# Performance work log

Hardware: AMD Instinct MI355X
Metric: run time of the kernel (lower is better)

Reference implementation:

```python
import jax, jax.numpy as jnp
import numpy as np
import math

HID = 512
HEADS = 8
DK = HID // HEADS
B, S, T = 8, 4096, 512


def setup_inputs() -> dict:
    key = jax.random.key(0)
    ks = jax.random.split(key, 12)
    scale = 0.02
    inp = {
        "inputs": jax.random.normal(ks[0], (B, S, HID), dtype=jnp.float32),
        "targets": jax.random.normal(ks[1], (B, T, HID), dtype=jnp.float32),
        "mask": jnp.ones((B, S), dtype=bool),
        "Wq": jax.random.normal(ks[2], (HID, HID), dtype=jnp.float32) * scale,
        "bq": jnp.zeros((HID,), dtype=jnp.float32),
        "Wk": jax.random.normal(ks[3], (HID, HID), dtype=jnp.float32) * scale,
        "bk": jnp.zeros((HID,), dtype=jnp.float32),
        "Wv": jax.random.normal(ks[4], (HID, HID), dtype=jnp.float32) * scale,
        "bv": jnp.zeros((HID,), dtype=jnp.float32),
        "Wo": jax.random.normal(ks[5], (HID, HID), dtype=jnp.float32) * scale,
        "bo": jnp.zeros((HID,), dtype=jnp.float32),
    }
    return inp


def reference(inputs, targets, mask, Wq, bq, Wk, bk, Wv, bv, Wo, bo):
    # PoolingFunction(method='multihead-attention'), dropout=0 (identity),
    # hidden_size == output_size so mapping_function is identity.
    b, t, h = targets.shape
    s = inputs.shape[1]
    Q = (targets @ Wq.T + bq).reshape(b, t, HEADS, DK)
    K = (inputs @ Wk.T + bk).reshape(b, s, HEADS, DK)
    V = (inputs @ Wv.T + bv).reshape(b, s, HEADS, DK)
    # scores: b x heads x tgt x seq (same math as (Q*K).sum(-1)/sqrt(d_k))
    e = jnp.einsum('bthd,bshd->bhts', Q, K) / math.sqrt(DK)
    neg = (1.0 - mask.astype(jnp.float32)) * -1e20  # b x s
    e = e + neg[:, None, None, :]
    a = jax.nn.softmax(e, axis=-1)  # softmax over seq dim
    ctx = jnp.einsum('bhts,bshd->bthd', a, V).reshape(b, t, h)
    return ctx @ Wo.T + bo
```

## Files before the change

### kernel.cpp

```cpp
#include <hip/hip_runtime.h>
#include <hip/hip_bf16.h>
#include <cstdint>
#include <cstddef>

#define HIDN   512
#define NHEADS 8
#define BATCH  8
#define SLEN   4096
#define TLEN   512
#define SSPLIT 4
#define SCHUNK (SLEN / SSPLIT)
#define SCL2   0.18033688f

typedef __attribute__((ext_vector_type(8))) short   bf16x8;
typedef __attribute__((ext_vector_type(4))) float   f32x4;
typedef unsigned short u16;
typedef unsigned int   u32;

__device__ __forceinline__ u32 pkbf(float a, float b) {
    __hip_bfloat162 h = __float22bfloat162_rn(float2{a, b});
    union { __hip_bfloat162 h; u32 u; } un; un.h = h; return un.u;
}
__device__ __forceinline__ u32 pk2(float a, float b) {
    union { float f; u32 u; } ua, ub; ua.f = a; ub.f = b;
    return __builtin_amdgcn_perm(ub.u + 0x8000u, ua.u + 0x8000u, 0x07060302u);
}
__device__ __forceinline__ void gload_lds16(const u16* g, u16* l) {
    __builtin_amdgcn_global_load_lds(
        (const __attribute__((address_space(1))) u32*)g,
        (__attribute__((address_space(3))) u32*)l, 16, 0, 0);
}

__global__ __launch_bounds__(256) void cvt_all(
    const float* __restrict__ X, const float* __restrict__ Tg,
    const float* __restrict__ Wq, const float* __restrict__ Wk,
    const float* __restrict__ Wv, const float* __restrict__ Wo,
    const int* __restrict__ mask,
    u16* __restrict__ Xc, u16* __restrict__ Tc, u16* __restrict__ Wc,
    float* __restrict__ negf)
{
    int i4 = blockIdx.x * 256 + threadIdx.x;
    if (i4 >= 4980736) {
        int off = i4 - 4980736;
        int4 mv = ((const int4*)mask)[off];
        float4 nv;
        nv.x = mv.x ? 0.f : -1e30f; nv.y = mv.y ? 0.f : -1e30f;
        nv.z = mv.z ? 0.f : -1e30f; nv.w = mv.w ? 0.f : -1e30f;
        ((float4*)negf)[off] = nv;
        return;
    }
    const float* s; u16* d; long off;
    if (i4 < 4194304)      { s = X;  d = Xc; off = i4; }
    else if (i4 < 4718592) { s = Tg; d = Tc; off = i4 - 4194304; }
    else {
        int wi = i4 - 4718592; int widx = wi >> 16;
        s = (widx == 0) ? Wq : (widx == 1) ? Wk : (widx == 2) ? Wv : Wo;
        d = Wc + widx * 262144; off = wi & 65535;
    }
    float4 v = *(const float4*)(s + off * 4);
    uint2 o; o.x = pkbf(v.x, v.y); o.y = pkbf(v.z, v.w);
    *(uint2*)(d + off * 4) = o;
}

template<int MODE, int SEQ>
__global__ __launch_bounds__(256)
void gemm_bf16(const u16* __restrict__ A, const u16* __restrict__ Bw,
               const float* __restrict__ bias, void* __restrict__ Yv)
{
    __shared__ u16 As[128 * 32];
    __shared__ u16 Bs[128 * 32];
    const int tid = threadIdx.x;
    const int lane = tid & 63, w = tid >> 6;
    const int m = lane & 15, qd = lane >> 4;
    const int wm = w >> 1, wn = w & 1;
    const int m0 = blockIdx.y * 128, n0 = blockIdx.x * 128;

    f32x4 acc[4][4];
#pragma unroll
    for (int i = 0; i < 4; ++i)
#pragma unroll
        for (int j = 0; j < 4; ++j) acc[i][j] = (f32x4){0.f, 0.f, 0.f, 0.f};

    for (int k0 = 0; k0 < HIDN; k0 += 32) {
#pragma unroll
        for (int r = 0; r < 2; ++r) {
            const int f = tid + r * 256;
            const int row = f >> 2, c8 = (f & 3) * 8;
            const int fb = f & ~63;
            gload_lds16(A  + (size_t)(m0 + row) * HIDN + k0 + c8, As + fb * 8);
            gload_lds16(Bw + (size_t)(n0 + row) * HIDN + k0 + c8, Bs + fb * 8);
        }
        __syncthreads();
        bf16x8 af[4], bf[4];
#pragma unroll
        for (int t = 0; t < 4; ++t) {
            af[t] = *(bf16x8*)&As[(64 * wm + 16 * t + m) * 32 + 8 * qd];
            bf[t] = *(bf16x8*)&Bs[(64 * wn + 16 * t + m) * 32 + 8 * qd];
        }
#pragma unroll
        for (int ti = 0; ti < 4; ++ti)
#pragma unroll
            for (int tj = 0; tj < 4; ++tj)
                acc[ti][tj] = __builtin_amdgcn_mfma_f32_16x16x32_bf16(
                    af[ti], bf[tj], acc[ti][tj], 0, 0, 0);
        __syncthreads();
    }

#pragma unroll
    for (int ti = 0; ti < 4; ++ti) {
        const int gr0 = m0 + 64 * wm + 16 * ti + 4 * qd;
#pragma unroll
        for (int tj = 0; tj < 4; ++tj) {
            const int gcol = n0 + 64 * wn + 16 * tj + m;
            const float bv = bias[gcol];
            if (MODE == 0) {
                float* Y = (float*)Yv;
#pragma unroll
                for (int i = 0; i < 4; ++i)
                    Y[(size_t)(gr0 + i) * HIDN + gcol] = acc[ti][tj][i] + bv;
            } else {
                u16* Y = (u16*)Yv;
                const int b = gr0 / SEQ, h = gcol >> 6, d = gcol & 63;
                const int r = gr0 & (SEQ - 1);
                uint2 o;
                o.x = pkbf(acc[ti][tj][0] + bv, acc[ti][tj][1] + bv);
                o.y = pkbf(acc[ti][tj][2] + bv, acc[ti][tj][3] + bv);
                *(uint2*)&Y[(((size_t)(b * 8 + h)) * 64 + d) * SEQ + r] = o;
            }
        }
    }
}

template<int SEQ>
__global__ __launch_bounds__(256)
void gemm_wxT(const u16* __restrict__ Wm, const u16* __restrict__ X,
              const float* __restrict__ bias, u16* __restrict__ Y)
{
    __shared__ u16 As[128 * 32];
    __shared__ u16 Bs[128 * 32];
    const int tid = threadIdx.x;
    const int lane = tid & 63, w = tid >> 6;
    const int m = lane & 15, qd = lane >> 4;
    const int wm = w >> 1, wn = w & 1;
    const int m0 = blockIdx.y * 128, n0 = blockIdx.x * 128;

    f32x4 acc[4][4];
#pragma unroll
    for (int i = 0; i < 4; ++i)
#pragma unroll
        for (int j = 0; j < 4; ++j) acc[i][j] = (f32x4){0.f, 0.f, 0.f, 0.f};

    for (int k0 = 0; k0 < HIDN; k0 += 32) {
#pragma unroll
        for (int r = 0; r < 2; ++r) {
            const int f = tid + r * 256;
            const int row = f >> 2, c8 = (f & 3) * 8;
            const int fb = f & ~63;
            gload_lds16(Wm + (size_t)(m0 + row) * HIDN + k0 + c8, As + fb * 8);
            gload_lds16(X  + (size_t)(n0 + row) * HIDN + k0 + c8, Bs + fb * 8);
        }
        __syncthreads();
        bf16x8 af[4], bf[4];
#pragma unroll
        for (int t = 0; t < 4; ++t) {
            af[t] = *(bf16x8*)&As[(64 * wm + 16 * t + m) * 32 + 8 * qd];
            bf[t] = *(bf16x8*)&Bs[(64 * wn + 16 * t + m) * 32 + 8 * qd];
        }
#pragma unroll
        for (int ti = 0; ti < 4; ++ti)
#pragma unroll
            for (int tj = 0; tj < 4; ++tj)
                acc[ti][tj] = __builtin_amdgcn_mfma_f32_16x16x32_bf16(
                    af[ti], bf[tj], acc[ti][tj], 0, 0, 0);
        __syncthreads();
    }

#pragma unroll
    for (int ti = 0; ti < 4; ++ti) {
        const int o = m0 + 64 * wm + 16 * ti + 4 * qd;
        const float4 bv = *(const float4*)&bias[o];
        const int h = o >> 6, d0 = o & 63;
#pragma unroll
        for (int tj = 0; tj < 4; ++tj) {
            const int n = n0 + 64 * wn + 16 * tj + m;
            const int b = n / SEQ, r = n & (SEQ - 1);
            uint2 pk;
            pk.x = pkbf(acc[ti][tj][0] + bv.x, acc[ti][tj][1] + bv.y);
            pk.y = pkbf(acc[ti][tj][2] + bv.z, acc[ti][tj][3] + bv.w);
            *(uint2*)&Y[(((size_t)(b * 8 + h)) * SEQ + r) * 64 + d0] = pk;
        }
    }
}

__global__ __launch_bounds__(256, 2)
void attn_part(const u16* __restrict__ Q, const u16* __restrict__ K,
               const u16* __restrict__ Vt, const float* __restrict__ negf,
               float* __restrict__ Opart, float* __restrict__ lpart)
{
    __shared__ char Psh[32768];
    const int tid = threadIdx.x;
    const int lane = tid & 63, w = tid >> 6;
    const int m = lane & 15, qd = lane >> 4;
    const int ti = blockIdx.x, si = blockIdx.y, bh = blockIdx.z;
    const int b = bh >> 3;

    const u16* Qp = Q + ((size_t)bh * TLEN + ti * 256) * 64;
    const u16* Kp = K + (size_t)bh * SLEN * 64;
    const u16* Vp = Vt + (size_t)bh * 64 * SLEN;
    const float* np = negf + (size_t)b * SLEN;

    const int wb = w * 8192 + m * 128;
    int waddr[4], ra0[2], ra1[2];
#pragma unroll
    for (int st = 0; st < 4; ++st) waddr[st] = wb + (((4 * st + qd) ^ m) << 3);
#pragma unroll
    for (int ks = 0; ks < 2; ++ks) {
        const int u0 = 8 * ks + 2 * qd;
        ra0[ks] = wb + (((u0) ^ m) << 3);
        ra1[ks] = wb + (((u0 + 1) ^ m) << 3);
    }

    bf16x8 qf[4][2];
#pragma unroll
    for (int ts = 0; ts < 4; ++ts)
#pragma unroll
        for (int kh = 0; kh < 2; ++kh)
            qf[ts][kh] = *(const bf16x8*)(Qp + (64 * w + 16 * ts + m) * 64 +
                                          32 * kh + 8 * qd);

    f32x4 O[4][4];
#pragma unroll
    for (int ts = 0; ts < 4; ++ts)
#pragma unroll
        for (int dt = 0; dt < 4; ++dt) O[ts][dt] = (f32x4){0.f, 0.f, 0.f, 0.f};
    float lr[4] = {0.f, 0.f, 0.f, 0.f};

    const int s_beg = si * SCHUNK;
    const u16* kp = Kp + (size_t)(s_beg + m) * 64 + 8 * qd;
    const u16* vp0 = Vp + (size_t)m * SLEN + s_beg + 8 * qd;
    const u16* vp1 = vp0 + (size_t)16 * SLEN;
    const u16* vp2 = vp0 + (size_t)32 * SLEN;
    const u16* vp3 = vp0 + (size_t)48 * SLEN;
    const float* npp = np + s_beg + 4 * qd;

#pragma unroll 1
    for (int c = 0; c < SCHUNK; c += 64) {
        bf16x8 kf[4][2];
        kf[0][0] = *(const bf16x8*)(kp + 0);
        kf[0][1] = *(const bf16x8*)(kp + 32);
        kf[1][0] = *(const bf16x8*)(kp + 1024);
        kf[1][1] = *(const bf16x8*)(kp + 1056);
        kf[2][0] = *(const bf16x8*)(kp + 2048);
        kf[2][1] = *(const bf16x8*)(kp + 2080);
        kf[3][0] = *(const bf16x8*)(kp + 3072);
        kf[3][1] = *(const bf16x8*)(kp + 3104);
        float4 ng[4];
        ng[0] = *(const float4*)(npp + 0);
        ng[1] = *(const float4*)(npp + 16);
        ng[2] = *(const float4*)(npp + 32);
        ng[3] = *(const float4*)(npp + 48);
        bf16x8 vf[4][2];
        vf[0][0] = *(const bf16x8*)(vp0 + 0);
        vf[0][1] = *(const bf16x8*)(vp0 + 32);
        vf[1][0] = *(const bf16x8*)(vp1 + 0);
        vf[1][1] = *(const bf16x8*)(vp1 + 32);
        vf[2][0] = *(const bf16x8*)(vp2 + 0);
        vf[2][1] = *(const bf16x8*)(vp2 + 32);
        vf[3][0] = *(const bf16x8*)(vp3 + 0);
        vf[3][1] = *(const bf16x8*)(vp3 + 32);

#pragma unroll
        for (int ts = 0; ts < 4; ++ts) {
            f32x4 S[4];
#pragma unroll
            for (int st = 0; st < 4; ++st) {
                f32x4 cc = (f32x4){0.f, 0.f, 0.f, 0.f};
                cc = __builtin_amdgcn_mfma_f32_16x16x32_bf16(kf[st][0], qf[ts][0], cc, 0, 0, 0);
                cc = __builtin_amdgcn_mfma_f32_16x16x32_bf16(kf[st][1], qf[ts][1], cc, 0, 0, 0);
                S[st] = cc;
            }
            float ls = 0.f;
#pragma unroll
            for (int st = 0; st < 4; ++st) {
                const float p0 = exp2f(fmaf(S[st][0], SCL2, ng[st].x));
                const float p1 = exp2f(fmaf(S[st][1], SCL2, ng[st].y));
                const float p2 = exp2f(fmaf(S[st][2], SCL2, ng[st].z));
                const float p3 = exp2f(fmaf(S[st][3], SCL2, ng[st].w));
                ls += (p0 + p1) + (p2 + p3);
                *(uint2*)&Psh[waddr[st] + ts * 2048] =
                    make_uint2(pk2(p0, p1), pk2(p2, p3));
            }
            lr[ts] += ls;
#pragma unroll
            for (int ks = 0; ks < 2; ++ks) {
                const uint2 r0 = *(uint2*)&Psh[ra0[ks] + ts * 2048];
                const uint2 r1 = *(uint2*)&Psh[ra1[ks] + ts * 2048];
                union { uint4 u; bf16x8 v; } bu;
                bu.u = make_uint4(r0.x, r0.y, r1.x, r1.y);
                O[ts][0] = __builtin_amdgcn_mfma_f32_16x16x32_bf16(vf[0][ks], bu.v, O[ts][0], 0, 0, 0);
                O[ts][1] = __builtin_amdgcn_mfma_f32_16x16x32_bf16(vf[1][ks], bu.v, O[ts][1], 0, 0, 0);
                O[ts][2] = __builtin_amdgcn_mfma_f32_16x16x32_bf16(vf[2][ks], bu.v, O[ts][2], 0, 0, 0);
                O[ts][3] = __builtin_amdgcn_mfma_f32_16x16x32_bf16(vf[3][ks], bu.v, O[ts][3], 0, 0, 0);
            }
        }
        kp += 4096; vp0 += 64; vp1 += 64; vp2 += 64; vp3 += 64; npp += 64;
    }

#pragma unroll
    for (int ts = 0; ts < 4; ++ts) {
        float l = lr[ts];
        l += __shfl_xor(l, 16, 64);
        l += __shfl_xor(l, 32, 64);
        const int t = ti * 256 + 64 * w + 16 * ts + m;
        float* Ob = Opart + (((size_t)(si * 64 + bh)) * 512 + t) * 64;
#pragma unroll
        for (int dt = 0; dt < 4; ++dt)
            *(f32x4*)&Ob[16 * dt + 4 * qd] = O[ts][dt];
        if (qd == 0)
            lpart[((size_t)(si * 64 + bh)) * 512 + t] = l;
    }
}

__global__ __launch_bounds__(256)
void attn_combine(const float* __restrict__ Opart, const float* __restrict__ lpart,
                  u16* __restrict__ ctx)
{
    const int gid = blockIdx.x * 256 + threadIdx.x;
    const int d4 = gid & 15, t = (gid >> 4) & 511, bh = gid >> 13;
    const int b = bh >> 3, h = bh & 7;
    float4 o = {0.f, 0.f, 0.f, 0.f}; float l = 0.f;
#pragma unroll
    for (int si = 0; si < SSPLIT; ++si) {
        const size_t base = ((size_t)(si * 64 + bh)) * 512 + t;
        l += lpart[base];
        const float4 v = *(const float4*)(Opart + base * 64 + d4 * 4);
        o.x += v.x; o.y += v.y; o.z += v.z; o.w += v.w;
    }
    const float r = 1.f / l;
    uint2 pk; pk.x = pkbf(o.x * r, o.y * r); pk.y = pkbf(o.z * r, o.w * r);
    *(uint2*)&ctx[((size_t)(b * 512 + t)) * 512 + h * 64 + d4 * 4] = pk;
}

extern "C" void kernel_launch(void* const* d_in, const int* in_sizes, int n_in,
                              void* d_out, int out_size, void* d_ws, size_t ws_size,
                              hipStream_t stream)
{
    const float* inputs  = (const float*)d_in[0];
    const float* targets = (const float*)d_in[1];
    const int*   mask    = (const int*)d_in[2];
    const float* Wq = (const float*)d_in[3];
    const float* bq = (const float*)d_in[4];
    const float* Wk = (const float*)d_in[5];
    const float* bk = (const float*)d_in[6];
    const float* Wv = (const float*)d_in[7];
    const float* bv = (const float*)d_in[8];
    const float* Wo = (const float*)d_in[9];
    const float* bo = (const float*)d_in[10];

    char* ws = (char*)d_ws;
    u16*   Xc    = (u16*)(ws);
    u16*   Tc    = (u16*)(ws + 33554432);
    u16*   Wc    = (u16*)(ws + 37748736);
    float* negf  = (float*)(ws + 39845888);
    u16*   Qws   = (u16*)(ws + 39976960);
    u16*   Kws   = (u16*)(ws + 44171264);
    u16*   Vtws  = (u16*)(ws + 77725696);
    u16*   Cws   = (u16*)(ws + 111280128);
    float* Opart = (float*)(ws + 115474432);
    float* lpart = (float*)(ws + 149028864);

    cvt_all<<<19488, 256, 0, stream>>>(inputs, targets, Wq, Wk, Wv, Wo, mask,
                                       Xc, Tc, Wc, negf);

    gemm_wxT<TLEN><<<dim3(32, 4),  256, 0, stream>>>(Wc,          Tc, bq, Qws);
    gemm_wxT<SLEN><<<dim3(256, 4), 256, 0, stream>>>(Wc + 262144, Xc, bk, Kws);
    gemm_bf16<2, SLEN><<<dim3(4, 256), 256, 0, stream>>>(Xc, Wc + 524288, bv, Vtws);

    attn_part<<<dim3(2, SSPLIT, 64), 256, 0, stream>>>(Qws, Kws, Vtws, negf,
                                                       Opart, lpart);
    attn_combine<<<2048, 256, 0, stream>>>(Opart, lpart, Cws);

    gemm_bf16<0, TLEN><<<dim3(4, 32), 256, 0, stream>>>(Cws, Wc + 786432, bo,
                                                        (float*)d_out);
}
```

Baseline: 299.2 us.

## Fuse split-S attention and combine into one 1024-thread block with LDS reduction

New measurement: 351.2 us. 17.4% more time.

```diff
diff --git a/kernel.cpp b/kernel.cpp
--- a/kernel.cpp
+++ b/kernel.cpp
@@ -8,8 +8,6 @@
 #define BATCH  8
 #define SLEN   4096
 #define TLEN   512
-#define SSPLIT 4
-#define SCHUNK (SLEN / SSPLIT)
 #define SCL2   0.18033688f
 
 typedef __attribute__((ext_vector_type(8))) short   bf16x8;
@@ -192,50 +190,54 @@
     }
 }
 
-__global__ __launch_bounds__(256, 2)
-void attn_part(const u16* __restrict__ Q, const u16* __restrict__ K,
-               const u16* __restrict__ Vt, const float* __restrict__ negf,
-               float* __restrict__ Opart, float* __restrict__ lpart)
-{
-    __shared__ char Psh[32768];
+__global__ __launch_bounds__(1024, 4)
+void attn_fused(const u16* __restrict__ Q, const u16* __restrict__ K,
+                const u16* __restrict__ Vt, const float* __restrict__ negf,
+                u16* __restrict__ ctx)
+{
+    __shared__ char  Psh[16 * 4096];
+    __shared__ float comb[8][4][64][4];
+    __shared__ float lsh[4][32];
+
     const int tid = threadIdx.x;
     const int lane = tid & 63, w = tid >> 6;
+    const int sg = w >> 2, tw = w & 3;
     const int m = lane & 15, qd = lane >> 4;
-    const int ti = blockIdx.x, si = blockIdx.y, bh = blockIdx.z;
-    const int b = bh >> 3;
-
-    const u16* Qp = Q + ((size_t)bh * TLEN + ti * 256) * 64;
+    const int ti = blockIdx.x, bh = blockIdx.y;
+    const int b = bh >> 3, h = bh & 7;
+
+    const u16* Qp = Q + ((size_t)bh * TLEN + ti * 128) * 64;
     const u16* Kp = K + (size_t)bh * SLEN * 64;
     const u16* Vp = Vt + (size_t)bh * 64 * SLEN;
     const float* np = negf + (size_t)b * SLEN;
 
-    const int wb = w * 8192 + m * 128;
+    const int wb = w * 4096 + m * 128;
     int waddr[4], ra0[2], ra1[2];
 #pragma unroll
     for (int st = 0; st < 4; ++st) waddr[st] = wb + (((4 * st + qd) ^ m) << 3);
 #pragma unroll
     for (int ks = 0; ks < 2; ++ks) {
         const int u0 = 8 * ks + 2 * qd;
-        ra0[ks] = wb + (((u0) ^ m) << 3);
+        ra0[ks] = wb + ((u0 ^ m) << 3);
         ra1[ks] = wb + (((u0 + 1) ^ m) << 3);
     }
 
-    bf16x8 qf[4][2];
-#pragma unroll
-    for (int ts = 0; ts < 4; ++ts)
+    bf16x8 qf[2][2];
+#pragma unroll
+    for (int ts = 0; ts < 2; ++ts)
 #pragma unroll
         for (int kh = 0; kh < 2; ++kh)
-            qf[ts][kh] = *(const bf16x8*)(Qp + (64 * w + 16 * ts + m) * 64 +
+            qf[ts][kh] = *(const bf16x8*)(Qp + (tw * 32 + ts * 16 + m) * 64 +
                                           32 * kh + 8 * qd);
 
-    f32x4 O[4][4];
-#pragma unroll
-    for (int ts = 0; ts < 4; ++ts)
+    f32x4 O[2][4];
+#pragma unroll
+    for (int ts = 0; ts < 2; ++ts)
 #pragma unroll
         for (int dt = 0; dt < 4; ++dt) O[ts][dt] = (f32x4){0.f, 0.f, 0.f, 0.f};
-    float lr[4] = {0.f, 0.f, 0.f, 0.f};
-
-    const int s_beg = si * SCHUNK;
+    float lr[2] = {0.f, 0.f};
+
+    const int s_beg = sg * 1024;
     const u16* kp = Kp + (size_t)(s_beg + m) * 64 + 8 * qd;
     const u16* vp0 = Vp + (size_t)m * SLEN + s_beg + 8 * qd;
     const u16* vp1 = vp0 + (size_t)16 * SLEN;
@@ -244,7 +246,7 @@
     const float* npp = np + s_beg + 4 * qd;
 
 #pragma unroll 1
-    for (int c = 0; c < SCHUNK; c += 64) {
+    for (int c = 0; c < 1024; c += 64) {
         bf16x8 kf[4][2];
         kf[0][0] = *(const bf16x8*)(kp + 0);
         kf[0][1] = *(const bf16x8*)(kp + 32);
@@ -270,7 +272,7 @@
         vf[3][1] = *(const bf16x8*)(vp3 + 32);
 
 #pragma unroll
-        for (int ts = 0; ts < 4; ++ts) {
+        for (int ts = 0; ts < 2; ++ts) {
             f32x4 S[4];
 #pragma unroll
             for (int st = 0; st < 4; ++st) {
@@ -282,10 +284,10 @@
             float ls = 0.f;
 #pragma unroll
             for (int st = 0; st < 4; ++st) {
-                const float p0 = exp2f(fmaf(S[st][0], SCL2, ng[st].x));
-                const float p1 = exp2f(fmaf(S[st][1], SCL2, ng[st].y));
-                const float p2 = exp2f(fmaf(S[st][2], SCL2, ng[st].z));
-                const float p3 = exp2f(fmaf(S[st][3], SCL2, ng[st].w));
+                const float p0 = __builtin_amdgcn_exp2f(fmaf(S[st][0], SCL2, ng[st].x));
+                const float p1 = __builtin_amdgcn_exp2f(fmaf(S[st][1], SCL2, ng[st].y));
+                const float p2 = __builtin_amdgcn_exp2f(fmaf(S[st][2], SCL2, ng[st].z));
+                const float p3 = __builtin_amdgcn_exp2f(fmaf(S[st][3], SCL2, ng[st].w));
                 ls += (p0 + p1) + (p2 + p3);
                 *(uint2*)&Psh[waddr[st] + ts * 2048] =
                     make_uint2(pk2(p0, p1), pk2(p2, p3));
@@ -306,39 +308,53 @@
         kp += 4096; vp0 += 64; vp1 += 64; vp2 += 64; vp3 += 64; npp += 64;
     }
 
-#pragma unroll
-    for (int ts = 0; ts < 4; ++ts) {
+    float lt[2];
+#pragma unroll
+    for (int ts = 0; ts < 2; ++ts) {
         float l = lr[ts];
         l += __shfl_xor(l, 16, 64);
         l += __shfl_xor(l, 32, 64);
-        const int t = ti * 256 + 64 * w + 16 * ts + m;
-        float* Ob = Opart + (((size_t)(si * 64 + bh)) * 512 + t) * 64;
-#pragma unroll
-        for (int dt = 0; dt < 4; ++dt)
-            *(f32x4*)&Ob[16 * dt + 4 * qd] = O[ts][dt];
-        if (qd == 0)
-            lpart[((size_t)(si * 64 + bh)) * 512 + t] = l;
-    }
-}
-
-__global__ __launch_bounds__(256)
-void attn_combine(const float* __restrict__ Opart, const float* __restrict__ lpart,
-                  u16* __restrict__ ctx)
-{
-    const int gid = blockIdx.x * 256 + threadIdx.x;
-    const int d4 = gid & 15, t = (gid >> 4) & 511, bh = gid >> 13;
-    const int b = bh >> 3, h = bh & 7;
-    float4 o = {0.f, 0.f, 0.f, 0.f}; float l = 0.f;
-#pragma unroll
-    for (int si = 0; si < SSPLIT; ++si) {
-        const size_t base = ((size_t)(si * 64 + bh)) * 512 + t;
-        l += lpart[base];
-        const float4 v = *(const float4*)(Opart + base * 64 + d4 * 4);
-        o.x += v.x; o.y += v.y; o.z += v.z; o.w += v.w;
-    }
-    const float r = 1.f / l;
-    uint2 pk; pk.x = pkbf(o.x * r, o.y * r); pk.y = pkbf(o.z * r, o.w * r);
-    *(uint2*)&ctx[((size_t)(b * 512 + t)) * 512 + h * 64 + d4 * 4] = pk;
+        lt[ts] = l;
+    }
+#pragma unroll 1
+    for (int r = 1; r < 4; ++r) {
+        if (sg == r) {
+#pragma unroll
+            for (int ts = 0; ts < 2; ++ts)
+#pragma unroll
+                for (int dt = 0; dt < 4; ++dt)
+                    *(f32x4*)&comb[ts * 4 + dt][tw][lane][0] = O[ts][dt];
+            if (qd == 0) { lsh[tw][m] = lt[0]; lsh[tw][16 + m] = lt[1]; }
+        }
+        __syncthreads();
+        if (sg == 0) {
+#pragma unroll
+            for (int ts = 0; ts < 2; ++ts)
+#pragma unroll
+                for (int dt = 0; dt < 4; ++dt) {
+                    const f32x4 v = *(f32x4*)&comb[ts * 4 + dt][tw][lane][0];
+                    O[ts][dt] += v;
+                }
+            lt[0] += lsh[tw][m];
+            lt[1] += lsh[tw][16 + m];
+        }
+        __syncthreads();
+    }
+    if (sg == 0) {
+#pragma unroll
+        for (int ts = 0; ts < 2; ++ts) {
+            const float linv = 1.f / lt[ts];
+            const int t = ti * 128 + tw * 32 + ts * 16 + m;
+            u16* cp = ctx + ((size_t)(b * TLEN + t)) * HIDN + h * 64;
+#pragma unroll
+            for (int dt = 0; dt < 4; ++dt) {
+                uint2 o;
+                o.x = pkbf(O[ts][dt][0] * linv, O[ts][dt][1] * linv);
+                o.y = pkbf(O[ts][dt][2] * linv, O[ts][dt][3] * linv);
+                *(uint2*)&cp[16 * dt + 4 * qd] = o;
+            }
+        }
+    }
 }
 
 extern "C" void kernel_launch(void* const* d_in, const int* in_sizes, int n_in,
@@ -366,8 +382,6 @@
     u16*   Kws   = (u16*)(ws + 44171264);
     u16*   Vtws  = (u16*)(ws + 77725696);
     u16*   Cws   = (u16*)(ws + 111280128);
-    float* Opart = (float*)(ws + 115474432);
-    float* lpart = (float*)(ws + 149028864);
 
     cvt_all<<<19488, 256, 0, stream>>>(inputs, targets, Wq, Wk, Wv, Wo, mask,
                                        Xc, Tc, Wc, negf);
@@ -376,9 +390,7 @@
     gemm_wxT<SLEN><<<dim3(256, 4), 256, 0, stream>>>(Wc + 262144, Xc, bk, Kws);
     gemm_bf16<2, SLEN><<<dim3(4, 256), 256, 0, stream>>>(Xc, Wc + 524288, bv, Vtws);
 
-    attn_part<<<dim3(2, SSPLIT, 64), 256, 0, stream>>>(Qws, Kws, Vtws, negf,
-                                                       Opart, lpart);
-    attn_combine<<<2048, 256, 0, stream>>>(Opart, lpart, Cws);
+    attn_fused<<<dim3(4, 64), 1024, 0, stream>>>(Qws, Kws, Vtws, negf, Cws);
 
     gemm_bf16<0, TLEN><<<dim3(4, 32), 256, 0, stream>>>(Cws, Wc + 786432, bo,
                                                         (float*)d_out);
```

## Split each attention block's sequence chunk across two wave groups and reduce in LDS

Applied to the files above, without the earlier changes.

Result: slower. 718.7 us (+140.2%).

```diff
diff --git a/kernel.cpp b/kernel.cpp
--- a/kernel.cpp
+++ b/kernel.cpp
@@ -9,7 +9,6 @@
 #define SLEN   4096
 #define TLEN   512
 #define SSPLIT 4
-#define SCHUNK (SLEN / SSPLIT)
 #define SCL2   0.18033688f
 
 typedef __attribute__((ext_vector_type(8))) short   bf16x8;
@@ -192,14 +191,17 @@
     }
 }
 
-__global__ __launch_bounds__(256, 2)
-void attn_part(const u16* __restrict__ Q, const u16* __restrict__ K,
-               const u16* __restrict__ Vt, const float* __restrict__ negf,
-               float* __restrict__ Opart, float* __restrict__ lpart)
-{
-    __shared__ char Psh[32768];
+__global__ __launch_bounds__(512, 4)
+void attn_fused(const u16* __restrict__ Q, const u16* __restrict__ K,
+                const u16* __restrict__ Vt, const float* __restrict__ negf,
+                float* __restrict__ Opart, float* __restrict__ lpart)
+{
+    __shared__ char  Psh[65536];
+    __shared__ float lsh[4][64];
+
     const int tid = threadIdx.x;
     const int lane = tid & 63, w = tid >> 6;
+    const int sg = w >> 2, tw = w & 3;
     const int m = lane & 15, qd = lane >> 4;
     const int ti = blockIdx.x, si = blockIdx.y, bh = blockIdx.z;
     const int b = bh >> 3;
@@ -216,7 +218,7 @@
 #pragma unroll
     for (int ks = 0; ks < 2; ++ks) {
         const int u0 = 8 * ks + 2 * qd;
-        ra0[ks] = wb + (((u0) ^ m) << 3);
+        ra0[ks] = wb + ((u0 ^ m) << 3);
         ra1[ks] = wb + (((u0 + 1) ^ m) << 3);
     }
 
@@ -225,7 +227,7 @@
     for (int ts = 0; ts < 4; ++ts)
 #pragma unroll
         for (int kh = 0; kh < 2; ++kh)
-            qf[ts][kh] = *(const bf16x8*)(Qp + (64 * w + 16 * ts + m) * 64 +
+            qf[ts][kh] = *(const bf16x8*)(Qp + (tw * 64 + ts * 16 + m) * 64 +
                                           32 * kh + 8 * qd);
 
     f32x4 O[4][4];
@@ -235,7 +237,7 @@
         for (int dt = 0; dt < 4; ++dt) O[ts][dt] = (f32x4){0.f, 0.f, 0.f, 0.f};
     float lr[4] = {0.f, 0.f, 0.f, 0.f};
 
-    const int s_beg = si * SCHUNK;
+    const int s_beg = si * 1024 + sg * 512;
     const u16* kp = Kp + (size_t)(s_beg + m) * 64 + 8 * qd;
     const u16* vp0 = Vp + (size_t)m * SLEN + s_beg + 8 * qd;
     const u16* vp1 = vp0 + (size_t)16 * SLEN;
@@ -244,7 +246,7 @@
     const float* npp = np + s_beg + 4 * qd;
 
 #pragma unroll 1
-    for (int c = 0; c < SCHUNK; c += 64) {
+    for (int c = 0; c < 512; c += 64) {
         bf16x8 kf[4][2];
         kf[0][0] = *(const bf16x8*)(kp + 0);
         kf[0][1] = *(const bf16x8*)(kp + 32);
@@ -282,10 +284,10 @@
             float ls = 0.f;
 #pragma unroll
             for (int st = 0; st < 4; ++st) {
-                const float p0 = exp2f(fmaf(S[st][0], SCL2, ng[st].x));
-                const float p1 = exp2f(fmaf(S[st][1], SCL2, ng[st].y));
-                const float p2 = exp2f(fmaf(S[st][2], SCL2, ng[st].z));
-                const float p3 = exp2f(fmaf(S[st][3], SCL2, ng[st].w));
+                const float p0 = __builtin_amdgcn_exp2f(fmaf(S[st][0], SCL2, ng[st].x));
+                const float p1 = __builtin_amdgcn_exp2f(fmaf(S[st][1], SCL2, ng[st].y));
+                const float p2 = __builtin_amdgcn_exp2f(fmaf(S[st][2], SCL2, ng[st].z));
+                const float p3 = __builtin_amdgcn_exp2f(fmaf(S[st][3], SCL2, ng[st].w));
                 ls += (p0 + p1) + (p2 + p3);
                 *(uint2*)&Psh[waddr[st] + ts * 2048] =
                     make_uint2(pk2(p0, p1), pk2(p2, p3));
@@ -306,18 +308,43 @@
         kp += 4096; vp0 += 64; vp1 += 64; vp2 += 64; vp3 += 64; npp += 64;
     }
 
+    float lt[4];
 #pragma unroll
     for (int ts = 0; ts < 4; ++ts) {
         float l = lr[ts];
         l += __shfl_xor(l, 16, 64);
         l += __shfl_xor(l, 32, 64);
-        const int t = ti * 256 + 64 * w + 16 * ts + m;
-        float* Ob = Opart + (((size_t)(si * 64 + bh)) * 512 + t) * 64;
-#pragma unroll
-        for (int dt = 0; dt < 4; ++dt)
-            *(f32x4*)&Ob[16 * dt + 4 * qd] = O[ts][dt];
-        if (qd == 0)
-            lpart[((size_t)(si * 64 + bh)) * 512 + t] = l;
+        lt[ts] = l;
+    }
+    __syncthreads();
+    float* combf = (float*)Psh;
+    if (sg == 1) {
+#pragma unroll
+        for (int ts = 0; ts < 4; ++ts) {
+#pragma unroll
+            for (int dt = 0; dt < 4; ++dt)
+                *(f32x4*)&combf[tw * 4096 + ts * 1024 + dt * 256 + lane * 4] =
+                    O[ts][dt];
+            if (qd == 0) lsh[tw][ts * 16 + m] = lt[ts];
+        }
+    }
+    __syncthreads();
+    if (sg == 0) {
+#pragma unroll
+        for (int ts = 0; ts < 4; ++ts) {
+            const float lsum = lt[ts] + lsh[tw][ts * 16 + m];
+            const int t = ti * 256 + tw * 64 + ts * 16 + m;
+            float* Ob = Opart + (((size_t)(si * 64 + bh)) * 512 + t) * 64;
+#pragma unroll
+            for (int dt = 0; dt < 4; ++dt) {
+                const f32x4 v = *(f32x4*)&combf[tw * 4096 + ts * 1024 + dt * 256 + lane * 4];
+                f32x4 o = O[ts][dt];
+                o[0] += v[0]; o[1] += v[1]; o[2] += v[2]; o[3] += v[3];
+                *(f32x4*)&Ob[16 * dt + 4 * qd] = o;
+            }
+            if (qd == 0)
+                lpart[((size_t)(si * 64 + bh)) * 512 + t] = lsum;
+        }
     }
 }
 
@@ -376,8 +403,8 @@
     gemm_wxT<SLEN><<<dim3(256, 4), 256, 0, stream>>>(Wc + 262144, Xc, bk, Kws);
     gemm_bf16<2, SLEN><<<dim3(4, 256), 256, 0, stream>>>(Xc, Wc + 524288, bv, Vtws);
 
-    attn_part<<<dim3(2, SSPLIT, 64), 256, 0, stream>>>(Qws, Kws, Vtws, negf,
-                                                       Opart, lpart);
+    attn_fused<<<dim3(2, 4, 64), 512, 0, stream>>>(Qws, Kws, Vtws, negf,
+                                                   Opart, lpart);
     attn_combine<<<2048, 256, 0, stream>>>(Opart, lpart, Cws);
 
     gemm_bf16<0, TLEN><<<dim3(4, 32), 256, 0, stream>>>(Cws, Wc + 786432, bo,
```
